# Performance work log

Measured on AMD Instinct MI355X. Metric: run time of the kernel, lower is better.

Reference implementation:

```python
import jax, jax.numpy as jnp
import numpy as np

HEADS, DIM_HEAD, DIM = 12, 64, 768
H = W = 32
N = H * W
B = 4


def _ln(x, g, b, eps=1e-5):
    mu = x.mean(-1, keepdims=True)
    var = ((x - mu) ** 2).mean(-1, keepdims=True)
    return (x - mu) / jnp.sqrt(var + eps) * g + b


def _get_epipolar(k, src_c2w, target_c2w, h=H, w=W):
    # Faithful port of Epipolar_Attention.get_epipolar, without the (hw*hw,3) repeat
    # materialization (uses broadcasting for the pairwise cross product instead).
    b = k.shape[0]
    Wf = h * 16.0 / 9.0
    k = k.astype(jnp.float32)
    k = k.at[:, 0, :].multiply(Wf).at[:, 1, :].multiply(float(h))
    k = k.at[:, 0, 2].set(h / 2.0).at[:, 1, 2].set(h / 2.0)
    ii, jj = jnp.meshgrid(jnp.arange(h), jnp.arange(w), indexing='ij')
    # after the torch column swap: (col, row, 1)
    coords = jnp.stack([jj.ravel(), ii.ravel(), jnp.ones(h * w, jnp.int32)], axis=1).astype(jnp.float32)  # [hw,3]
    k3 = k[:, :3, :3]
    src_r, src_t = src_c2w[:, :3, :3].astype(jnp.float32), src_c2w[:, :3, 3].astype(jnp.float32)
    tgt_r, tgt_t = target_c2w[:, :3, :3].astype(jnp.float32), target_c2w[:, :3, 3].astype(jnp.float32)
    tgt_rinv = jnp.linalg.inv(tgt_r)
    fx, fy = k3[:, 0, 0][:, None], k3[:, 1, 1][:, None]
    cx, cy = k3[:, 0, 2][:, None], k3[:, 1, 2][:, None]
    nc = jnp.stack([(coords[None, :, 0] - cx) / fx,
                    (coords[None, :, 1] - cy) / fy,
                    jnp.broadcast_to(coords[None, :, 2], (b, h * w))], axis=-1)  # [b,hw,3]
    p3w = jnp.einsum('bij,bnj->bni', src_r, nc) + src_t[:, None]
    p2 = jnp.einsum('bij,bnj->bni', tgt_rinv, p3w) - tgt_t[:, None]  # target_w2c_t = -target_c2w_t
    pij_un = jnp.einsum('bij,bnj->bni', k3, p2)                      # [b,hw,3]
    pij = pij_un / (pij_un[..., -1:] + 1e-6)
    o2 = jnp.einsum('bij,bj->bi', tgt_rinv, src_t) - tgt_t           # origin projected
    oij = jnp.einsum('bij,bj->bi', k3, o2)
    oij = oij / oij[..., -1:]
    oi_to_pi = pij - oij[:, None]                # [b,hw,3]
    oi_to_coord = coords[None] - oij[:, None]    # [b,hw,3]
    cr = jnp.cross(oi_to_pi[:, :, None, :], oi_to_coord[:, None, :, :])  # [b,hw,hw,3]
    area = jnp.sqrt((cr * cr).sum(-1))
    vlen = jnp.sqrt((oi_to_pi * oi_to_pi).sum(-1))[:, :, None]
    dist = area / vlen
    dw = 1.0 - jax.nn.sigmoid(50.0 * (dist - 0.5))
    row_max = dw.max(-1, keepdims=True)
    return jnp.where(row_max < 0.5, 1.0, dw)     # rows with max<0.5 are set to all-ones


def setup_inputs():
    key = jax.random.key(0)
    ks = jax.random.split(key, 16)
    s = 0.02
    x = jax.random.normal(ks[0], (B, N, DIM), jnp.float32)
    src_encode = jax.random.normal(ks[1], (B, N, DIM), jnp.float32)
    intrinsic = (jnp.zeros((B, 4, 4), jnp.float32)
                 .at[:, 0, 0].set(1.0).at[:, 1, 1].set(1.0)
                 .at[:, 0, 2].set(0.5).at[:, 1, 2].set(0.5)
                 .at[:, 2, 2].set(1.0).at[:, 3, 3].set(1.0))
    R = jnp.eye(3, dtype=jnp.float32) + 0.1 * jax.random.normal(ks[2], (2, B, 3, 3), jnp.float32)
    t = 0.5 * jax.random.normal(ks[3], (2, B, 3), jnp.float32)
    c2w = (jnp.zeros((2, B, 4, 4), jnp.float32)
           .at[:, :, :3, :3].set(R).at[:, :, :3, 3].set(t).at[:, :, 3, 3].set(1.0))
    hd = HEADS * DIM_HEAD
    w_ = lambda k_, shp: s * jax.random.normal(k_, shp, jnp.float32)
    return dict(
        x=x, src_encode=src_encode, intrinsic=intrinsic, c2w=c2w,
        lnq_g=jnp.ones(DIM), lnq_b=jnp.zeros(DIM), Wq=w_(ks[4], (DIM, hd)), bq=jnp.zeros(hd),
        lnk_g=jnp.ones(DIM), lnk_b=jnp.zeros(DIM), Wk=w_(ks[5], (DIM, hd)), bk=jnp.zeros(hd),
        lnv_g=jnp.ones(DIM), lnv_b=jnp.zeros(DIM), Wv=w_(ks[6], (DIM, hd)), bv=jnp.zeros(hd),
        Wp=w_(ks[7], (hd, DIM)), bp=jnp.zeros(DIM),
        pre_g=jnp.ones(DIM), pre_b=jnp.zeros(DIM),
        W1=w_(ks[8], (DIM, 2 * DIM)), b1=jnp.zeros(2 * DIM),
        W2=w_(ks[9], (2 * DIM, DIM)), b2=jnp.zeros(DIM),
        post_g=jnp.ones(DIM), post_b=jnp.zeros(DIM))


def reference(x, src_encode, intrinsic, c2w, lnq_g, lnq_b, Wq, bq, lnk_g, lnk_b, Wk, bk,
              lnv_g, lnv_b, Wv, bv, Wp, bp, pre_g, pre_b, W1, b1, W2, b2, post_g, post_b):
    b, n, _ = x.shape
    scale = DIM_HEAD ** -0.5
    split = lambda t_: t_.reshape(b, n, HEADS, DIM_HEAD).transpose(0, 2, 1, 3)  # [b,m,n,d]
    q = split(_ln(x, lnq_g, lnq_b) @ Wq + bq)
    k = split(_ln(src_encode, lnk_g, lnk_b) @ Wk + bk)
    v = split(_ln(src_encode, lnv_g, lnv_b) @ Wv + bv)
    scores = scale * jnp.einsum('bmqd,bmkd->bmqk', q, k)
    e1 = _get_epipolar(intrinsic, c2w[1], c2w[0])                    # do_epipolar
    e2 = jnp.swapaxes(_get_epipolar(intrinsic, c2w[0], c2w[1]), 1, 2)  # bidirectional (transposed)
    wmap = e1 * e2                                                   # [b,n,n], shared across heads
    att = jax.nn.softmax(scores * wmap[:, None], axis=-1)
    a = jnp.einsum('bmqk,bmkd->bmqd', att, v).transpose(0, 2, 1, 3).reshape(b, n, HEADS * DIM_HEAD)
    z = _ln(a @ Wp + bp, pre_g, pre_b)
    z = z + (jax.nn.gelu(z @ W1 + b1, approximate=False) @ W2 + b2)  # torch nn.GELU = exact erf
    z = _ln(z, post_g, post_b)
    wm_full = jnp.broadcast_to(wmap[:, None], (b, HEADS, n, n)).reshape(b * HEADS, n, n)
    return z, wm_full
```

## Files before the change

### kernel.cpp

```cpp
#include <hip/hip_runtime.h>
#include <hip/hip_bf16.h>

typedef unsigned short u16;
typedef __attribute__((ext_vector_type(4))) unsigned short u16x4;
typedef __attribute__((ext_vector_type(8))) unsigned short u16x8;
typedef __attribute__((ext_vector_type(8))) short s16x8;
typedef __attribute__((ext_vector_type(4))) float f32x4;

#define HEADS 12
#define NSEQ 1024
#define DIMM 768
#define DHEAD 64

__device__ __forceinline__ float b2f(u16 h) {
  union { unsigned u; float f; } v; v.u = ((unsigned)h) << 16; return v.f;
}
__device__ __forceinline__ u16 f2b(float f) {
  union { float f; unsigned u; } v; v.f = f;
  unsigned r = v.u + 0x7fffu + ((v.u >> 16) & 1u);
  return (u16)(r >> 16);
}
__device__ __forceinline__ void gl_lds16(const u16* g, u16* l) {
  __builtin_amdgcn_global_load_lds(
      (const __attribute__((address_space(1))) void*)g,
      (__attribute__((address_space(3))) void*)l, 16, 0, 0);
}

template<bool GELU, bool RESID, bool VTOUT>
__device__ __forceinline__ void gemm64(
    const u16* __restrict__ A, const u16* __restrict__ BT,
    const float* __restrict__ bias, const u16* __restrict__ resid,
    const float* __restrict__ rg, const float* __restrict__ rb,
    u16* __restrict__ C, int K, int lda, int ldb, int ldc,
    int m0, int n0, u16* As, u16* Bs, u16* __restrict__ vt)
{
  const int tid = threadIdx.x;
  const int lane = tid & 63;
  const int wv = tid >> 6;
  const int wm0 = (wv >> 1) * 32;
  const int wn0 = (wv & 1) * 32;
  const int l15 = lane & 15;
  const int quad = lane >> 4;
  const int srow = lane >> 2;
  const int scol = (lane & 3) * 8;

  f32x4 acc[2][2];
  #pragma unroll
  for (int i = 0; i < 2; ++i)
    #pragma unroll
    for (int j = 0; j < 2; ++j)
      acc[i][j] = {0.f, 0.f, 0.f, 0.f};

  const u16* Ab = A + (long)(m0 + wv * 16 + srow) * lda + scol;
  const u16* Bb = BT + (long)(n0 + wv * 16 + srow) * ldb + scol;
  u16* AsW = As + (wv * 16) * 32;
  u16* BsW = Bs + (wv * 16) * 32;

  auto issue = [&](int buf, int kk) {
    gl_lds16(Ab + kk, AsW + buf * 2048);
    gl_lds16(Bb + kk, BsW + buf * 2048);
  };

  const int NK = K >> 5;
  issue(0, 0);
  issue(1, 32);

  int cur = 0;
  for (int i = 0; i < NK; ++i) {
    if (i + 1 < NK) asm volatile("s_waitcnt vmcnt(2)" ::: "memory");
    else            asm volatile("s_waitcnt vmcnt(0)" ::: "memory");
    __builtin_amdgcn_s_barrier();
    __builtin_amdgcn_sched_barrier(0);
    if (i + 2 < NK) {
      int nb = cur + 2; if (nb >= 3) nb -= 3;
      issue(nb, (i + 2) * 32);
    }
    const u16* Ac = As + cur * 2048;
    const u16* Bc = Bs + cur * 2048;
    s16x8 af[2], bfr[2];
    #pragma unroll
    for (int i2 = 0; i2 < 2; ++i2)
      af[i2] = *(const s16x8*)&Ac[(wm0 + i2 * 16 + l15) * 32 + quad * 8];
    #pragma unroll
    for (int j = 0; j < 2; ++j)
      bfr[j] = *(const s16x8*)&Bc[(wn0 + j * 16 + l15) * 32 + quad * 8];
    #pragma unroll
    for (int i2 = 0; i2 < 2; ++i2)
      #pragma unroll
      for (int j = 0; j < 2; ++j)
        acc[i2][j] = __builtin_amdgcn_mfma_f32_16x16x32_bf16(af[i2], bfr[j], acc[i2][j], 0, 0, 0);
    ++cur; if (cur == 3) cur = 0;
  }

  if (VTOUT) {
    __syncthreads();
    u16* shp = As;
    const int b = m0 >> 10;
    const int nloc = m0 & 1023;
    const int fb0 = n0 - 768;
    #pragma unroll
    for (int j = 0; j < 2; ++j) {
      const float bvv = bias[n0 + wn0 + j * 16 + l15];
      #pragma unroll
      for (int i = 0; i < 2; ++i)
        #pragma unroll
        for (int v = 0; v < 4; ++v)
          shp[(wm0 + i * 16 + quad * 4 + v) * 72 + (wn0 + j * 16 + l15)] =
              f2b(acc[i][j][v] + bvv);
    }
    __syncthreads();
    const int f = tid >> 2;
    const int nb = (tid & 3) * 16;
    u16x8 o0, o1;
    #pragma unroll
    for (int nn = 0; nn < 8; ++nn) {
      o0[nn] = shp[(nb + nn) * 72 + f];
      o1[nn] = shp[(nb + 8 + nn) * 72 + f];
    }
    u16* dst = vt + ((long)(b * 768 + fb0 + f)) * NSEQ + nloc + nb;
    *(u16x8*)&dst[0] = o0;
    *(u16x8*)&dst[8] = o1;
    return;
  }

  #pragma unroll
  for (int i = 0; i < 2; ++i)
    #pragma unroll
    for (int j = 0; j < 2; ++j) {
      const int col = n0 + wn0 + j * 16 + l15;
      const float bvv = bias[col];
      #pragma unroll
      for (int v = 0; v < 4; ++v) {
        const int row = m0 + wm0 + i * 16 + quad * 4 + v;
        float val = acc[i][j][v] + bvv;
        if (GELU) val = 0.5f * val * (1.0f + erff(val * 0.70710678118654752440f));
        if (RESID) val += b2f(resid[(long)row * ldc + col]) * rg[col] + rb[col];
        C[(long)row * ldc + col] = f2b(val);
      }
    }
}

template<bool GELU, bool RESID>
__global__ __launch_bounds__(256)
void gemm_one(const u16* __restrict__ A, const u16* __restrict__ BT,
              const float* __restrict__ bias, const u16* __restrict__ resid,
              const float* __restrict__ rg, const float* __restrict__ rb,
              u16* __restrict__ C, int K, int lda, int ldb, int ldc)
{
  __shared__ u16 As[6144], Bs[6144];
  gemm64<GELU, RESID, false>(A, BT, bias, resid, rg, rb, C, K, lda, ldb, ldc,
                             blockIdx.x * 64, blockIdx.y * 64, As, Bs, nullptr);
}

__device__ __forceinline__ float dwval(f32x4 U, float ox, float oy, float oz, int m)
{
  const float cx = (float)(m & 31) - ox;
  const float cy = (float)(m >> 5) - oy;
  const float cz = 1.0f - oz;
  const float crx = U.y * cz - U.z * cy;
  const float cry = U.z * cx - U.x * cz;
  const float crz = U.x * cy - U.y * cx;
  const float area = sqrtf(crx * crx + cry * cry + crz * crz);
  const float dist = area / U.w;
  const float t = 50.0f * (dist - 0.5f);
  return 1.0f - 1.0f / (1.0f + __expf(-t));
}

#define PREP_T0 13824
#define PREP_T1 14016
#define PREP_T2 22208
#define PREP_T3 30400

__global__ __launch_bounds__(256)
void prep2(const float* w0, const float* w1, const float* w2,
           const float* w3, const float* w4, const float* w5,
           const float* gq, const float* gk, const float* gv, const float* gp,
           u16* d0, u16* d12, u16* d3, u16* d4, u16* d5,
           const float* bq, const float* bk, const float* bv, const float* b1,
           const float* lnqb, const float* lnkb, const float* lnvb, const float* preb,
           float* obq, float* obkv, float* ob1,
           const float* intr, const float* c2w,
           float* u4, float* oijb, float* flags,
           const float* nx, const float* nsrc, u16* onx, u16* onsrc)
{
  const int bid = blockIdx.x;
  const int tid = threadIdx.x;

  if (bid < PREP_T0) {
    __shared__ u16 t[32][36];
    const int z = bid / 2304;
    const int rem = bid - z * 2304;
    const int bx = rem % 48, by = rem / 48;
    const float* src; const float* g; u16* dst; int R, C; float sc = 1.0f;
    switch (z) {
      case 0: src = w0; g = gq; dst = d0;  R = 768;  C = 768;  sc = 0.125f; break;
      case 1: src = w1; g = gk; dst = d12; R = 768;  C = 768;  break;
      case 2: src = w2; g = gv; dst = d12 + 768 * 768; R = 768; C = 768; break;
      case 3: src = w3; g = nullptr; dst = d3; R = 768;  C = 768;  break;
      case 4: src = w4; g = gp; dst = d4; R = 768;  C = 1536; break;
      default: src = w5; g = nullptr; dst = d5; R = 1536; C = 768; break;
    }
    const int c0 = bx * 32;
    const int r0 = by * 32;
    if (c0 >= C || r0 >= R) return;
    const int i = tid >> 3;
    const int j4 = (tid & 7) * 4;
    const float rs = (g ? g[r0 + i] : 1.0f) * sc;
    #pragma unroll
    for (int jj = 0; jj < 4; ++jj)
      t[i][j4 + jj] = f2b(src[(long)(r0 + i) * C + c0 + j4 + jj] * rs);
    __syncthreads();
    u16x4 ov;
    #pragma unroll
    for (int jj = 0; jj < 4; ++jj) ov[jj] = t[j4 + jj][i];
    *(u16x4*)&dst[(long)(c0 + i) * R + r0 + j4] = ov;
    return;
  }

  if (bid < PREP_T1) {
    __shared__ float red[8][32];
    const int idx = bid - PREP_T0;
    const int y = idx / 48;
    const int bx = idx % 48;
    const float* W; const float* bln; const float* bw; float* out;
    int C; float sc = 1.0f;
    switch (y) {
      case 0: W = w0; bln = lnqb; bw = bq; out = obq;        C = 768;  sc = 0.125f; break;
      case 1: W = w1; bln = lnkb; bw = bk; out = obkv;       C = 768;  break;
      case 2: W = w2; bln = lnvb; bw = bv; out = obkv + 768; C = 768;  break;
      default: W = w4; bln = preb; bw = b1; out = ob1;       C = 1536; break;
    }
    const int c0 = bx * 32;
    if (c0 >= C) return;
    const int cl = tid & 31;
    const int rg = tid >> 5;
    const int c = c0 + cl;
    float s = 0.f;
    for (int r = rg * 96; r < rg * 96 + 96; ++r)
      s += bln[r] * W[(long)r * C + c];
    red[rg][cl] = s;
    __syncthreads();
    if (rg == 0) {
      float tot = bw[c];
      #pragma unroll
      for (int k = 0; k < 8; ++k) tot += red[k][cl];
      out[c] = tot * sc;
    }
    return;
  }

  if (bid < PREP_T2) {
    __shared__ float S[40];
    __shared__ float redf[8];
    const int rowid = bid - PREP_T1;
    const int db = rowid >> 10;
    const int n = rowid & 1023;
    const int d = db >> 2, b = db & 3;
    if (tid == 0) {
      const int sidx = (d == 0) ? 1 : 0;
      const int tidx = 1 - sidx;
      float k3[9], sr[9], st[3], tr[9], tt[3];
      const float Wf = 32.0f * 16.0f / 9.0f;
      for (int j = 0; j < 3; ++j) {
        k3[j]     = intr[(b * 4 + 0) * 4 + j] * Wf;
        k3[3 + j] = intr[(b * 4 + 1) * 4 + j] * 32.0f;
        k3[6 + j] = intr[(b * 4 + 2) * 4 + j];
      }
      k3[2] = 16.0f; k3[5] = 16.0f;
      for (int i = 0; i < 3; ++i) {
        for (int j = 0; j < 3; ++j) {
          sr[i * 3 + j] = c2w[((sidx * 4 + b) * 4 + i) * 4 + j];
          tr[i * 3 + j] = c2w[((tidx * 4 + b) * 4 + i) * 4 + j];
        }
        st[i] = c2w[((sidx * 4 + b) * 4 + i) * 4 + 3];
        tt[i] = c2w[((tidx * 4 + b) * 4 + i) * 4 + 3];
      }
      double a = tr[0], bb_ = tr[1], c = tr[2];
      double dd2 = tr[3], e = tr[4], f = tr[5];
      double g2 = tr[6], h2 = tr[7], i2 = tr[8];
      double det = a * (e * i2 - f * h2) - bb_ * (dd2 * i2 - f * g2) + c * (dd2 * h2 - e * g2);
      double inv[9] = {
        (e * i2 - f * h2), (c * h2 - bb_ * i2), (bb_ * f - c * e),
        (f * g2 - dd2 * i2), (a * i2 - c * g2), (c * dd2 - a * f),
        (dd2 * h2 - e * g2), (bb_ * g2 - a * h2), (a * e - bb_ * dd2)
      };
      float tri[9];
      for (int t2 = 0; t2 < 9; ++t2) tri[t2] = (float)(inv[t2] / det);
      float o2[3], oij[3];
      for (int i3 = 0; i3 < 3; ++i3)
        o2[i3] = tri[i3 * 3] * st[0] + tri[i3 * 3 + 1] * st[1] + tri[i3 * 3 + 2] * st[2] - tt[i3];
      for (int i3 = 0; i3 < 3; ++i3)
        oij[i3] = k3[i3 * 3] * o2[0] + k3[i3 * 3 + 1] * o2[1] + k3[i3 * 3 + 2] * o2[2];
      const float ozf = oij[2];
      oij[0] = oij[0] / ozf; oij[1] = oij[1] / ozf; oij[2] = ozf / ozf;
      if (n == 0) {
        oijb[db * 4 + 0] = oij[0]; oijb[db * 4 + 1] = oij[1];
        oijb[db * 4 + 2] = oij[2]; oijb[db * 4 + 3] = 0.f;
      }
      const float ncx = ((float)(n & 31) - k3[2]) / k3[0];
      const float ncy = ((float)(n >> 5) - k3[5]) / k3[4];
      const float p0 = sr[0] * ncx + sr[1] * ncy + sr[2] + st[0];
      const float p1 = sr[3] * ncx + sr[4] * ncy + sr[5] + st[1];
      const float p2 = sr[6] * ncx + sr[7] * ncy + sr[8] + st[2];
      const float q0 = tri[0] * p0 + tri[1] * p1 + tri[2] * p2 - tt[0];
      const float q1 = tri[3] * p0 + tri[4] * p1 + tri[5] * p2 - tt[1];
      const float q2 = tri[6] * p0 + tri[7] * p1 + tri[8] * p2 - tt[2];
      const float ww0 = k3[0] * q0 + k3[1] * q1 + k3[2] * q2;
      const float ww1 = k3[3] * q0 + k3[4] * q1 + k3[5] * q2;
      const float ww2 = k3[6] * q0 + k3[7] * q1 + k3[8] * q2;
      const float pz = ww2 + 1e-6f;
      const float ux = ww0 / pz - oij[0];
      const float uy = ww1 / pz - oij[1];
      const float uz = ww2 / pz - oij[2];
      const float vlen = sqrtf(ux * ux + uy * uy + uz * uz);
      f32x4 uo = {ux, uy, uz, vlen};
      *(f32x4*)&u4[(long)rowid * 4] = uo;
      S[33] = oij[0]; S[34] = oij[1]; S[35] = oij[2];
      S[36] = ux; S[37] = uy; S[38] = uz; S[39] = vlen;
    }
    __syncthreads();
    const f32x4 U = {S[36], S[37], S[38], S[39]};
    const float ox = S[33], oy = S[34], oz = S[35];
    float mx = -1e30f;
    #pragma unroll
    for (int i = 0; i < 4; ++i)
      mx = fmaxf(mx, dwval(U, ox, oy, oz, tid + i * 256));
    #pragma unroll
    for (int off = 32; off; off >>= 1) mx = fmaxf(mx, __shfl_down(mx, off));
    const int lane = tid & 63, wid = tid >> 6;
    if (!lane) redf[wid] = mx;
    __syncthreads();
    if (!tid) {
      const float m4 = fmaxf(fmaxf(redf[0], redf[1]), fmaxf(redf[2], redf[3]));
      flags[rowid] = (m4 < 0.5f) ? 1.0f : 0.0f;
    }
    return;
  }

  {
    __shared__ float s1[8], s2[8];
    const int r = bid - PREP_T2;
    const float* p = ((r < 4096) ? nx : nsrc) + (long)(r & 4095) * DIMM;
    u16* o = ((r < 4096) ? onx : onsrc) + (long)(r & 4095) * DIMM;
    float v0 = p[tid], v1 = p[tid + 256], v2 = p[tid + 512];
    float s = v0 + v1 + v2;
    #pragma unroll
    for (int off = 32; off; off >>= 1) s += __shfl_down(s, off);
    const int lane = tid & 63, wid = tid >> 6;
    if (!lane) s1[wid] = s;
    __syncthreads();
    if (!tid) s1[4] = s1[0] + s1[1] + s1[2] + s1[3];
    __syncthreads();
    const float mu = s1[4] / 768.0f;
    float d0 = v0 - mu, d1 = v1 - mu, d2 = v2 - mu;
    float sq = d0 * d0 + d1 * d1 + d2 * d2;
    #pragma unroll
    for (int off = 32; off; off >>= 1) sq += __shfl_down(sq, off);
    if (!lane) s2[wid] = sq;
    __syncthreads();
    if (!tid) s2[4] = s2[0] + s2[1] + s2[2] + s2[3];
    __syncthreads();
    const float rstd = 1.0f / sqrtf(s2[4] / 768.0f + 1e-5f);
    o[tid]       = f2b(d0 * rstd);
    o[tid + 256] = f2b(d1 * rstd);
    o[tid + 512] = f2b(d2 * rstd);
  }
}

__global__ __launch_bounds__(256)
void stageB(const u16* __restrict__ nx, const u16* __restrict__ ns,
            const u16* __restrict__ qT, const u16* __restrict__ kvT,
            const float* __restrict__ bqf, const float* __restrict__ bkvf,
            u16* __restrict__ qb, u16* __restrict__ kvb, u16* __restrict__ vT,
            const float* __restrict__ u4, const float* __restrict__ oijb,
            const float* __restrict__ flags,
            u16* __restrict__ wm, float* __restrict__ wm_full)
{
  __shared__ __align__(16) u16 sh[12288];
  const int bid = blockIdx.x;
  const int tid = threadIdx.x;

  if (bid < 2304) {
    u16* As = sh;
    u16* Bs = sh + 6144;
    const int z = bid / 768;
    const int idx = bid - z * 768;
    const int x = idx & 63;
    const int y = idx >> 6;
    if (z == 0)
      gemm64<false, false, false>(nx, qT, bqf, nullptr, nullptr, nullptr, qb,
                                  768, 768, 768, 768,
                                  x * 64, y * 64, As, Bs, nullptr);
    else if (z == 1)
      gemm64<false, false, false>(ns, kvT, bkvf, nullptr, nullptr, nullptr, kvb,
                                  768, 768, 768, 1536,
                                  x * 64, y * 64, As, Bs, nullptr);
    else
      gemm64<false, false, true>(ns, kvT, bkvf, nullptr, nullptr, nullptr, nullptr,
                                 768, 768, 768, 1536,
                                 x * 64, 768 + y * 64, As, Bs, vT);
    return;
  }

  const int id = bid - 2304;
  const int qx = id & 31;
  const int ky = (id >> 5) & 31;
  const int b = id >> 10;
  const int q0 = qx * 32;
  const int k0 = ky * 32;
  const int i = tid >> 3;
  const int j4 = (tid & 7) * 4;

  f32x4* U2s = (f32x4*)sh;
  float* f2s = (float*)(sh + 256);
  float* f1s = (float*)(sh + 320);
  if (tid < 32) {
    U2s[tid] = *(const f32x4*)&u4[((long)(4 + b) * 1024 + k0 + tid) * 4];
    f2s[tid] = flags[(4 + b) * 1024 + k0 + tid];
    f1s[tid] = flags[b * 1024 + q0 + tid];
  }
  __syncthreads();

  const int q = q0 + i;
  const f32x4 U1 = *(const f32x4*)&u4[((long)b * 1024 + q) * 4];
  const float o1x = oijb[b * 4 + 0], o1y = oijb[b * 4 + 1], o1z = oijb[b * 4 + 2];
  const float o2x = oijb[(4 + b) * 4 + 0], o2y = oijb[(4 + b) * 4 + 1], o2z = oijb[(4 + b) * 4 + 2];
  const bool fl1 = f1s[i] > 0.5f;

  u16x4 pk;
  f32x4 wf;
  #pragma unroll
  for (int jj = 0; jj < 4; ++jj) {
    const int k = k0 + j4 + jj;
    const float e1 = fl1 ? 1.0f : dwval(U1, o1x, o1y, o1z, k);
    const float e2 = (f2s[j4 + jj] > 0.5f) ? 1.0f : dwval(U2s[j4 + jj], o2x, o2y, o2z, q);
    const float w = e1 * e2;
    wf[jj] = w;
    pk[jj] = f2b(w);
  }
  *(u16x4*)&wm[((long)b * 1024 + q0 + i) * 1024 + k0 + j4] = pk;
  #pragma unroll
  for (int h = 0; h < HEADS; ++h)
    *(f32x4*)&wm_full[((long)(b * HEADS + h) * 1024 + q0 + i) * 1024 + k0 + j4] = wf;
}

__global__ __launch_bounds__(256, 3)
void fattn(const u16* __restrict__ qb, const u16* __restrict__ kvb,
           const u16* __restrict__ vT, const u16* __restrict__ wm,
           u16* __restrict__ outA)
{
  __shared__ u16 Qs[2 * 64 * 32];
  __shared__ u16 Ks[2][2 * 64 * 32];
  __shared__ u16 Vs[2][2 * 64 * 32];
  __shared__ u16 Ps[64][72];

  const int bh = blockIdx.y;
  const int b = bh / HEADS, h = bh - b * HEADS;
  const int q0 = blockIdx.x * 64;
  const int tid = threadIdx.x;
  const int lane = tid & 63;
  const int wv = tid >> 6;
  const int l15 = lane & 15;
  const int quad = lane >> 4;
  const int srow = lane >> 2;
  const int scol = (lane & 3) * 8;

  const u16* Qg = qb + ((long)b * NSEQ + q0) * DIMM + h * DHEAD;
  const u16* Kg = kvb + (long)b * NSEQ * 1536 + h * DHEAD;
  const u16* Vg = vT + (long)bh * DHEAD * NSEQ;
  const u16* Wg = wm + ((long)b * NSEQ + q0) * NSEQ;

  #pragma unroll
  for (int h2 = 0; h2 < 2; ++h2) {
    gl_lds16(Qg + (long)(wv * 16 + srow) * DIMM + h2 * 32 + scol,
             Qs + (h2 * 64 + wv * 16) * 32);
    gl_lds16(Kg + (long)(wv * 16 + srow) * 1536 + h2 * 32 + scol,
             Ks[0] + (h2 * 64 + wv * 16) * 32);
    gl_lds16(Vg + (long)(wv * 16 + srow) * NSEQ + h2 * 32 + scol,
             Vs[0] + (h2 * 64 + wv * 16) * 32);
  }

  f32x4 Sacc[4], Oacc[4];
  float mrow[4], lrow[4];
  #pragma unroll
  for (int j = 0; j < 4; ++j) {
    Oacc[j] = {0.f, 0.f, 0.f, 0.f};
    mrow[j] = -3.0e38f;
    lrow[j] = 0.f;
  }
  s16x8 qf[2];

  int cur = 0;
  for (int kt = 0; kt < 16; ++kt) {
    __syncthreads();
    if (kt < 15) {
      const int nxt = cur ^ 1;
      #pragma unroll
      for (int h2 = 0; h2 < 2; ++h2) {
        gl_lds16(Kg + (long)((kt + 1) * 64 + wv * 16 + srow) * 1536 + h2 * 32 + scol,
                 Ks[nxt] + (h2 * 64 + wv * 16) * 32);
        gl_lds16(Vg + (long)(wv * 16 + srow) * NSEQ + (kt + 1) * 64 + h2 * 32 + scol,
                 Vs[nxt] + (h2 * 64 + wv * 16) * 32);
      }
    }

    if (kt == 0) {
      qf[0] = *(const s16x8*)&Qs[(0 * 64 + wv * 16 + l15) * 32 + quad * 8];
      qf[1] = *(const s16x8*)&Qs[(1 * 64 + wv * 16 + l15) * 32 + quad * 8];
    }

    float wr[4][4];
    #pragma unroll
    for (int j = 0; j < 4; ++j)
      #pragma unroll
      for (int v = 0; v < 4; ++v)
        wr[j][v] = b2f(Wg[(long)(wv * 16 + quad * 4 + v) * NSEQ + kt * 64 + j * 16 + l15]);

    #pragma unroll
    for (int j = 0; j < 4; ++j) Sacc[j] = {0.f, 0.f, 0.f, 0.f};
    #pragma unroll
    for (int j = 0; j < 4; ++j)
      #pragma unroll
      for (int h2 = 0; h2 < 2; ++h2) {
        s16x8 kf = *(const s16x8*)&Ks[cur][(h2 * 64 + j * 16 + l15) * 32 + quad * 8];
        Sacc[j] = __builtin_amdgcn_mfma_f32_16x16x32_bf16(qf[h2], kf, Sacc[j], 0, 0, 0);
      }

    #pragma unroll
    for (int j = 0; j < 4; ++j)
      #pragma unroll
      for (int v = 0; v < 4; ++v)
        Sacc[j][v] *= wr[j][v];
    #pragma unroll
    for (int v = 0; v < 4; ++v) {
      float tm = fmaxf(fmaxf(Sacc[0][v], Sacc[1][v]), fmaxf(Sacc[2][v], Sacc[3][v]));
      tm = fmaxf(tm, __shfl_xor(tm, 1));
      tm = fmaxf(tm, __shfl_xor(tm, 2));
      tm = fmaxf(tm, __shfl_xor(tm, 4));
      tm = fmaxf(tm, __shfl_xor(tm, 8));
      const float mnew = fmaxf(mrow[v], tm);
      const float al = __expf(mrow[v] - mnew);
      float rs = 0.f;
      #pragma unroll
      for (int j = 0; j < 4; ++j) {
        const float e = __expf(Sacc[j][v] - mnew);
        Sacc[j][v] = e;
        rs += e;
      }
      rs += __shfl_xor(rs, 1);
      rs += __shfl_xor(rs, 2);
      rs += __shfl_xor(rs, 4);
      rs += __shfl_xor(rs, 8);
      lrow[v] = lrow[v] * al + rs;
      mrow[v] = mnew;
      #pragma unroll
      for (int jn = 0; jn < 4; ++jn) Oacc[jn][v] *= al;
    }
    #pragma unroll
    for (int j = 0; j < 4; ++j)
      #pragma unroll
      for (int v = 0; v < 4; ++v)
        Ps[wv * 16 + quad * 4 + v][j * 16 + l15] = f2b(Sacc[j][v]);

    #pragma unroll
    for (int h2 = 0; h2 < 2; ++h2) {
      s16x8 af = *(const s16x8*)&Ps[wv * 16 + l15][h2 * 32 + quad * 8];
      #pragma unroll
      for (int jn = 0; jn < 4; ++jn) {
        s16x8 vf = *(const s16x8*)&Vs[cur][(h2 * 64 + jn * 16 + l15) * 32 + quad * 8];
        Oacc[jn] = __builtin_amdgcn_mfma_f32_16x16x32_bf16(af, vf, Oacc[jn], 0, 0, 0);
      }
    }
    cur ^= 1;
  }

  #pragma unroll
  for (int v = 0; v < 4; ++v) {
    const int row = q0 + wv * 16 + quad * 4 + v;
    const float inv = 1.0f / lrow[v];
    #pragma unroll
    for (int jn = 0; jn < 4; ++jn)
      outA[((long)(b * NSEQ + row)) * DIMM + h * DHEAD + jn * 16 + l15] =
          f2b(Oacc[jn][v] * inv);
  }
}

__global__ __launch_bounds__(256)
void norm_k(const u16* __restrict__ in, u16* __restrict__ out)
{
  const long base = (long)blockIdx.x * DIMM;
  const int tid = threadIdx.x;
  __shared__ float s1[8], s2[8];
  const u16* p = in + base;
  float v0 = b2f(p[tid]), v1 = b2f(p[tid + 256]), v2 = b2f(p[tid + 512]);
  float s = v0 + v1 + v2;
  #pragma unroll
  for (int off = 32; off; off >>= 1) s += __shfl_down(s, off);
  const int lane = tid & 63, wid = tid >> 6;
  if (!lane) s1[wid] = s;
  __syncthreads();
  if (!tid) s1[4] = s1[0] + s1[1] + s1[2] + s1[3];
  __syncthreads();
  const float mu = s1[4] / 768.0f;
  float d0 = v0 - mu, d1 = v1 - mu, d2 = v2 - mu;
  float sq = d0 * d0 + d1 * d1 + d2 * d2;
  #pragma unroll
  for (int off = 32; off; off >>= 1) sq += __shfl_down(sq, off);
  if (!lane) s2[wid] = sq;
  __syncthreads();
  if (!tid) s2[4] = s2[0] + s2[1] + s2[2] + s2[3];
  __syncthreads();
  const float rstd = 1.0f / sqrtf(s2[4] / 768.0f + 1e-5f);
  u16* o = out + base;
  o[tid]       = f2b(d0 * rstd);
  o[tid + 256] = f2b(d1 * rstd);
  o[tid + 512] = f2b(d2 * rstd);
}

__global__ __launch_bounds__(256)
void ln_final(const u16* __restrict__ in, const float* __restrict__ g,
              const float* __restrict__ bb, float* __restrict__ out)
{
  const long base = (long)blockIdx.x * DIMM;
  const int tid = threadIdx.x;
  __shared__ float s1[8], s2[8];
  const u16* p = in + base;
  float v0 = b2f(p[tid]), v1 = b2f(p[tid + 256]), v2 = b2f(p[tid + 512]);
  float s = v0 + v1 + v2;
  #pragma unroll
  for (int off = 32; off; off >>= 1) s += __shfl_down(s, off);
  const int lane = tid & 63, wid = tid >> 6;
  if (!lane) s1[wid] = s;
  __syncthreads();
  if (!tid) s1[4] = s1[0] + s1[1] + s1[2] + s1[3];
  __syncthreads();
  const float mu = s1[4] / 768.0f;
  float d0 = v0 - mu, d1 = v1 - mu, d2 = v2 - mu;
  float sq = d0 * d0 + d1 * d1 + d2 * d2;
  #pragma unroll
  for (int off = 32; off; off >>= 1) sq += __shfl_down(sq, off);
  if (!lane) s2[wid] = sq;
  __syncthreads();
  if (!tid) s2[4] = s2[0] + s2[1] + s2[2] + s2[3];
  __syncthreads();
  const float rstd = 1.0f / sqrtf(s2[4] / 768.0f + 1e-5f);
  float* o = out + base;
  o[tid]       = d0 * rstd * g[tid]       + bb[tid];
  o[tid + 256] = d1 * rstd * g[tid + 256] + bb[tid + 256];
  o[tid + 512] = d2 * rstd * g[tid + 512] + bb[tid + 512];
}

extern "C" void kernel_launch(void* const* d_in, const int* in_sizes, int n_in,
                              void* d_out, int out_size, void* d_ws, size_t ws_size,
                              hipStream_t stream)
{
  (void)in_sizes; (void)n_in; (void)out_size; (void)ws_size;
  const float* x     = (const float*)d_in[0];
  const float* src   = (const float*)d_in[1];
  const float* intr  = (const float*)d_in[2];
  const float* c2w   = (const float*)d_in[3];
  const float* lnq_g = (const float*)d_in[4];
  const float* lnq_b = (const float*)d_in[5];
  const float* Wq    = (const float*)d_in[6];
  const float* bq    = (const float*)d_in[7];
  const float* lnk_g = (const float*)d_in[8];
  const float* lnk_b = (const float*)d_in[9];
  const float* Wk    = (const float*)d_in[10];
  const float* bk    = (const float*)d_in[11];
  const float* lnv_g = (const float*)d_in[12];
  const float* lnv_b = (const float*)d_in[13];
  const float* Wv    = (const float*)d_in[14];
  const float* bv    = (const float*)d_in[15];
  const float* Wp    = (const float*)d_in[16];
  const float* bp    = (const float*)d_in[17];
  const float* pre_g = (const float*)d_in[18];
  const float* pre_b = (const float*)d_in[19];
  const float* W1    = (const float*)d_in[20];
  const float* b1    = (const float*)d_in[21];
  const float* W2    = (const float*)d_in[22];
  const float* b2    = (const float*)d_in[23];
  const float* post_g= (const float*)d_in[24];
  const float* post_b= (const float*)d_in[25];

  char* ws = (char*)d_ws;
  size_t off = 0;
  auto alloc = [&](size_t bytes) -> char* {
    char* p = ws + off;
    off = (off + bytes + 255) & ~(size_t)255;
    return p;
  };
  const size_t SEQD = (size_t)4096 * 768 * 2;

  u16* WqT  = (u16*)alloc(768 * 768 * 2);
  u16* WkvT = (u16*)alloc((size_t)1536 * 768 * 2);
  u16* WpT  = (u16*)alloc(768 * 768 * 2);
  u16* W1T  = (u16*)alloc(768 * 1536 * 2);
  u16* W2T  = (u16*)alloc(1536 * 768 * 2);
  float* bqf  = (float*)alloc(768 * 4);
  float* bkvf = (float*)alloc(1536 * 4);
  float* b1f  = (float*)alloc(1536 * 4);
  char* pool = alloc(6 * SEQD);
  float* u4   = (float*)alloc(8 * 1024 * 4 * 4);
  float* oijb = (float*)alloc(8 * 4 * 4);
  u16* wmapb  = (u16*)alloc((size_t)4 * 1024 * 1024 * 2);
  float* flagb = (float*)alloc(8 * 1024 * 4);

  u16* S0 = (u16*)pool;
  u16* S1 = (u16*)(pool + SEQD);
  u16* S2 = (u16*)(pool + 2 * SEQD);
  u16* S3 = (u16*)(pool + 3 * SEQD);
  u16* S5 = (u16*)(pool + 5 * SEQD);

  float* out_z  = (float*)d_out;
  float* out_wm = (float*)d_out + (size_t)4 * 1024 * 768;

  prep2<<<PREP_T3, 256, 0, stream>>>(
      Wq, Wk, Wv, Wp, W1, W2, lnq_g, lnk_g, lnv_g, pre_g,
      WqT, WkvT, WpT, W1T, W2T,
      bq, bk, bv, b1, lnq_b, lnk_b, lnv_b, pre_b,
      bqf, bkvf, b1f,
      intr, c2w, u4, oijb, flagb,
      x, src, S0, S1);

  stageB<<<6400, 256, 0, stream>>>(
      S0, S1, WqT, WkvT, bqf, bkvf, S2, S3, S5,
      u4, oijb, flagb, wmapb, out_wm);

  fattn<<<dim3(16, 48), 256, 0, stream>>>(S2, S3, S5, wmapb, S0);

  gemm_one<false, false><<<dim3(64, 12), 256, 0, stream>>>(
      S0, WpT, bp, nullptr, nullptr, nullptr, S1, 768, 768, 768, 768);

  norm_k<<<4096, 256, 0, stream>>>(S1, S2);

  gemm_one<true, false><<<dim3(64, 24), 256, 0, stream>>>(
      S2, W1T, b1f, nullptr, nullptr, nullptr, S3, 768, 768, 768, 1536);

  gemm_one<false, true><<<dim3(64, 12), 256, 0, stream>>>(
      S3, W2T, b2, S2, pre_g, pre_b, S5, 1536, 1536, 1536, 768);

  ln_final<<<4096, 256, 0, stream>>>(S5, post_g, post_b, out_z);
}
```

Measured before the change: 480.4 us.

## Swizzle LDS layouts and deepen GEMM K-tile to 64 to cut bank conflicts

The shared GEMM routine now stages 64-wide K tiles, with two 32-row sub-loads per wave, in an XOR-swizzled LDS layout. Fragment reads use the matching swizzle, which avoids bank conflicts and halves the number of barrier-synchronised iterations. The flash-attention kernel applies a similar XOR swizzle to its Q/K/V staging and fragment reads. The cost is double the LDS footprint per block in the GEMM kernels, which may lower occupancy, plus more outstanding loads per wait.

```diff
diff --git a/kernel.cpp b/kernel.cpp
--- a/kernel.cpp
+++ b/kernel.cpp
@@ -41,8 +41,9 @@
   const int wn0 = (wv & 1) * 32;
   const int l15 = lane & 15;
   const int quad = lane >> 4;
-  const int srow = lane >> 2;
-  const int scol = (lane & 3) * 8;
+  const int srow = wv * 8 + (lane >> 3);
+  const int schunk = lane & 7;
+  const int scol = (schunk ^ (srow & 7)) * 8;
 
   f32x4 acc[2][2];
   #pragma unroll
@@ -51,44 +52,50 @@
     for (int j = 0; j < 2; ++j)
       acc[i][j] = {0.f, 0.f, 0.f, 0.f};
 
-  const u16* Ab = A + (long)(m0 + wv * 16 + srow) * lda + scol;
-  const u16* Bb = BT + (long)(n0 + wv * 16 + srow) * ldb + scol;
-  u16* AsW = As + (wv * 16) * 32;
-  u16* BsW = Bs + (wv * 16) * 32;
+  const u16* Ab = A + (long)(m0 + srow) * lda + scol;
+  const u16* Bb = BT + (long)(n0 + srow) * ldb + scol;
 
   auto issue = [&](int buf, int kk) {
-    gl_lds16(Ab + kk, AsW + buf * 2048);
-    gl_lds16(Bb + kk, BsW + buf * 2048);
+    #pragma unroll
+    for (int s = 0; s < 2; ++s) {
+      gl_lds16(Ab + kk + (long)s * 32 * lda, As + buf * 4096 + s * 2048 + wv * 512);
+      gl_lds16(Bb + kk + (long)s * 32 * ldb, Bs + buf * 4096 + s * 2048 + wv * 512);
+    }
   };
 
-  const int NK = K >> 5;
+  const int NK = K >> 6;
   issue(0, 0);
-  issue(1, 32);
+  issue(1, 64);
 
   int cur = 0;
   for (int i = 0; i < NK; ++i) {
-    if (i + 1 < NK) asm volatile("s_waitcnt vmcnt(2)" ::: "memory");
+    if (i + 1 < NK) asm volatile("s_waitcnt vmcnt(4)" ::: "memory");
     else            asm volatile("s_waitcnt vmcnt(0)" ::: "memory");
     __builtin_amdgcn_s_barrier();
     __builtin_amdgcn_sched_barrier(0);
     if (i + 2 < NK) {
       int nb = cur + 2; if (nb >= 3) nb -= 3;
-      issue(nb, (i + 2) * 32);
-    }
-    const u16* Ac = As + cur * 2048;
-    const u16* Bc = Bs + cur * 2048;
-    s16x8 af[2], bfr[2];
-    #pragma unroll
-    for (int i2 = 0; i2 < 2; ++i2)
-      af[i2] = *(const s16x8*)&Ac[(wm0 + i2 * 16 + l15) * 32 + quad * 8];
-    #pragma unroll
-    for (int j = 0; j < 2; ++j)
-      bfr[j] = *(const s16x8*)&Bc[(wn0 + j * 16 + l15) * 32 + quad * 8];
-    #pragma unroll
-    for (int i2 = 0; i2 < 2; ++i2)
+      issue(nb, (i + 2) * 64);
+    }
+    const u16* Ac = As + cur * 4096;
+    const u16* Bc = Bs + cur * 4096;
+    #pragma unroll
+    for (int kk = 0; kk < 2; ++kk) {
+      s16x8 af[2], bfr[2];
+      #pragma unroll
+      for (int i2 = 0; i2 < 2; ++i2)
+        af[i2] = *(const s16x8*)&Ac[(wm0 + i2 * 16 + l15) * 64 +
+                                    (((kk * 4 + quad) ^ (l15 & 7)) * 8)];
       #pragma unroll
       for (int j = 0; j < 2; ++j)
-        acc[i2][j] = __builtin_amdgcn_mfma_f32_16x16x32_bf16(af[i2], bfr[j], acc[i2][j], 0, 0, 0);
+        bfr[j] = *(const s16x8*)&Bc[(wn0 + j * 16 + l15) * 64 +
+                                    (((kk * 4 + quad) ^ (l15 & 7)) * 8)];
+      #pragma unroll
+      for (int i2 = 0; i2 < 2; ++i2)
+        #pragma unroll
+        for (int j = 0; j < 2; ++j)
+          acc[i2][j] = __builtin_amdgcn_mfma_f32_16x16x32_bf16(af[i2], bfr[j], acc[i2][j], 0, 0, 0);
+    }
     ++cur; if (cur == 3) cur = 0;
   }
 
@@ -147,7 +154,7 @@
               const float* __restrict__ rg, const float* __restrict__ rb,
               u16* __restrict__ C, int K, int lda, int ldb, int ldc)
 {
-  __shared__ u16 As[6144], Bs[6144];
+  __shared__ u16 As[12288], Bs[12288];
   gemm64<GELU, RESID, false>(A, BT, bias, resid, rg, rb, C, K, lda, ldb, ldc,
                              blockIdx.x * 64, blockIdx.y * 64, As, Bs, nullptr);
 }
@@ -376,13 +383,13 @@
             const float* __restrict__ flags,
             u16* __restrict__ wm, float* __restrict__ wm_full)
 {
-  __shared__ __align__(16) u16 sh[12288];
+  __shared__ __align__(16) u16 sh[24576];
   const int bid = blockIdx.x;
   const int tid = threadIdx.x;
 
   if (bid < 2304) {
     u16* As = sh;
-    u16* Bs = sh + 6144;
+    u16* Bs = sh + 12288;
     const int z = bid / 768;
     const int idx = bid - z * 768;
     const int x = idx & 63;
@@ -463,7 +470,8 @@
   const int l15 = lane & 15;
   const int quad = lane >> 4;
   const int srow = lane >> 2;
-  const int scol = (lane & 3) * 8;
+  const int sscol = ((lane & 3) ^ (srow & 3)) * 8;
+  const int rch = (quad ^ (l15 & 3)) * 8;
 
   const u16* Qg = qb + ((long)b * NSEQ + q0) * DIMM + h * DHEAD;
   const u16* Kg = kvb + (long)b * NSEQ * 1536 + h * DHEAD;
@@ -472,11 +480,11 @@
 
   #pragma unroll
   for (int h2 = 0; h2 < 2; ++h2) {
-    gl_lds16(Qg + (long)(wv * 16 + srow) * DIMM + h2 * 32 + scol,
+    gl_lds16(Qg + (long)(wv * 16 + srow) * DIMM + h2 * 32 + sscol,
              Qs + (h2 * 64 + wv * 16) * 32);
-    gl_lds16(Kg + (long)(wv * 16 + srow) * 1536 + h2 * 32 + scol,
+    gl_lds16(Kg + (long)(wv * 16 + srow) * 1536 + h2 * 32 + sscol,
              Ks[0] + (h2 * 64 + wv * 16) * 32);
-    gl_lds16(Vg + (long)(wv * 16 + srow) * NSEQ + h2 * 32 + scol,
+    gl_lds16(Vg + (long)(wv * 16 + srow) * NSEQ + h2 * 32 + sscol,
              Vs[0] + (h2 * 64 + wv * 16) * 32);
   }
 
@@ -497,16 +505,16 @@
       const int nxt = cur ^ 1;
       #pragma unroll
       for (int h2 = 0; h2 < 2; ++h2) {
-        gl_lds16(Kg + (long)((kt + 1) * 64 + wv * 16 + srow) * 1536 + h2 * 32 + scol,
+        gl_lds16(Kg + (long)((kt + 1) * 64 + wv * 16 + srow) * 1536 + h2 * 32 + sscol,
                  Ks[nxt] + (h2 * 64 + wv * 16) * 32);
-        gl_lds16(Vg + (long)(wv * 16 + srow) * NSEQ + (kt + 1) * 64 + h2 * 32 + scol,
+        gl_lds16(Vg + (long)(wv * 16 + srow) * NSEQ + (kt + 1) * 64 + h2 * 32 + sscol,
                  Vs[nxt] + (h2 * 64 + wv * 16) * 32);
       }
     }
 
     if (kt == 0) {
-      qf[0] = *(const s16x8*)&Qs[(0 * 64 + wv * 16 + l15) * 32 + quad * 8];
-      qf[1] = *(const s16x8*)&Qs[(1 * 64 + wv * 16 + l15) * 32 + quad * 8];
+      qf[0] = *(const s16x8*)&Qs[(0 * 64 + wv * 16 + l15) * 32 + rch];
+      qf[1] = *(const s16x8*)&Qs[(1 * 64 + wv * 16 + l15) * 32 + rch];
     }
 
     float wr[4][4];
@@ -522,7 +530,7 @@
     for (int j = 0; j < 4; ++j)
       #pragma unroll
       for (int h2 = 0; h2 < 2; ++h2) {
-        s16x8 kf = *(const s16x8*)&Ks[cur][(h2 * 64 + j * 16 + l15) * 32 + quad * 8];
+        s16x8 kf = *(const s16x8*)&Ks[cur][(h2 * 64 + j * 16 + l15) * 32 + rch];
         Sacc[j] = __builtin_amdgcn_mfma_f32_16x16x32_bf16(qf[h2], kf, Sacc[j], 0, 0, 0);
       }
 
@@ -567,7 +575,7 @@
       s16x8 af = *(const s16x8*)&Ps[wv * 16 + l15][h2 * 32 + quad * 8];
       #pragma unroll
       for (int jn = 0; jn < 4; ++jn) {
-        s16x8 vf = *(const s16x8*)&Vs[cur][(h2 * 64 + jn * 16 + l15) * 32 + quad * 8];
+        s16x8 vf = *(const s16x8*)&Vs[cur][(h2 * 64 + jn * 16 + l15) * 32 + rch];
         Oacc[jn] = __builtin_amdgcn_mfma_f32_16x16x32_bf16(af, vf, Oacc[jn], 0, 0, 0);
       }
     }
```

Measured after the change: 461.2 us. 1.04x faster.
